# Performance work log

Hardware: AMD Instinct MI355X
Metric: run time of the kernel (lower is better)

Reference implementation:

```python
import jax, jax.numpy as jnp
import numpy as np

ATOL = 1e-06
RTOL = 1e-06

def setup_inputs() -> dict:
    key = jax.random.key(0)
    ks = jax.random.split(key, 8)
    u = lambda k, shape: jax.random.uniform(k, shape, jnp.float32, -0.05, 0.05)
    return {
        "x": jax.random.normal(ks[0], (4096, 32, 32, 3), jnp.float32),
        "W_lstm": u(ks[1], (3, 16)),      # input kernel, gates [i,f,c,o]
        "U_lstm": u(ks[2], (4, 16)),      # recurrent kernel
        "dw_kernel": u(ks[3], (27, 27, 3, 5)),  # depthwise (kh,kw,in_c,mult)
        "pw_kernel": u(ks[4], (15, 4)),   # pointwise
        "conv_bias": u(ks[5], (4,)),
        "W_td": u(ks[6], (4096, 10)),
        "W_sc": u(ks[7], (4096, 10)),
    }

def _lstm_td(x, W, U):
    # TimeDistributed LSTM: x (B,32,32,3) -> treat axis1 as TD batch, axis2 as time
    B = x.shape[0]
    seq = x.reshape(B * 32, 32, 3)          # (N, T, F)
    xs = jnp.transpose(seq, (1, 0, 2))      # (T, N, F)
    N = seq.shape[0]
    h0 = jnp.zeros((N, 4), x.dtype)
    c0 = jnp.zeros((N, 4), x.dtype)

    def step(carry, xt):
        h, c = carry
        z = xt @ W + h @ U                  # (N, 16)
        zi, zf, zc, zo = jnp.split(z, 4, axis=-1)
        i = jax.nn.elu(zi)                  # recurrent_activation='elu'
        f = jax.nn.elu(zf)
        c = f * c + i * jax.nn.softmax(zc, axis=-1)  # activation='softmax'
        o = jax.nn.elu(zo)
        h = o * jax.nn.softmax(c, axis=-1)
        return (h, c), h

    _, hs = jax.lax.scan(step, (h0, c0), xs)        # (T, N, 4)
    return jnp.transpose(hs, (1, 0, 2)).reshape(B, 32, 32, 4)

def _sep_conv(x, dw_kernel, pw_kernel, conv_bias):
    # depthwise: Keras (kh,kw,C,M) -> lax HWIO grouped (kh,kw,1,C*M), channel-major order
    dw = dw_kernel.reshape(27, 27, 1, 15)
    y = jax.lax.conv_general_dilated(
        x, dw, window_strides=(1, 1), padding='SAME',
        feature_group_count=3,
        dimension_numbers=('NHWC', 'HWIO', 'NHWC'))   # (B,32,32,15)
    y = jnp.einsum('bhwc,cf->bhwf', y, pw_kernel) + conv_bias
    return jax.nn.sigmoid(y)                          # (B,32,32,4)

def reference(x, W_lstm, U_lstm, dw_kernel, pw_kernel, conv_bias, W_td, W_sc):
    B = x.shape[0]
    td = _lstm_td(x, W_lstm, U_lstm).reshape(B, -1) @ W_td   # (B,10)
    sc = _sep_conv(x, dw_kernel, pw_kernel, conv_bias).reshape(B, -1) @ W_sc
    diff = jnp.abs(td - sc)
    tol = ATOL + RTOL * jnp.abs(sc)
    return diff <= tol
```

## Files before the change

### kernel.cpp

```cpp
#include <hip/hip_runtime.h>
#include <math.h>

#define TD_OFF 0
#define WTDR_OFF 40960
#define SC_OFF 81920
#define BG_BYTE_OFF 524288

typedef __bf16 bf16x8 __attribute__((ext_vector_type(8)));
typedef float f32x16 __attribute__((ext_vector_type(16)));

union FragU { bf16x8 v; float4 f; };

__device__ __forceinline__ f32x16 mfma16(bf16x8 a, bf16x8 b, f32x16 c) {
    return __builtin_amdgcn_mfma_f32_32x32x16_bf16(a, b, c, 0, 0, 0);
}

__device__ __forceinline__ float eluf(float v) {
    return v > 0.f ? v : __expf(v) - 1.f;
}

__global__ __launch_bounds__(256) void prep(const float* __restrict__ dw,
                                            const float* __restrict__ pw,
                                            const float* __restrict__ Wtd,
                                            float* __restrict__ Wtdr,
                                            unsigned short* __restrict__ Bg) {
    int gid = blockIdx.x * 256 + threadIdx.x;
    if (gid < 40960) {
        int k = gid & 3;
        int r = gid >> 2;
        int row = r & 31; r >>= 5;
        int j = r % 10;
        int tt = r / 10;
        Wtdr[gid] = Wtd[(size_t)(row * 128 + tt * 4 + k) * 10 + j];
        return;
    }
    int g2 = gid - 40960;
    if (g2 >= 162 * 128) return;
    int n = g2 & 127;
    int s = g2 >> 7;
    int half = s & 1;
    int cd = s >> 1;
    int c = cd / 27, d = cd % 27;
    int w = n >> 2, f = n & 3;
    unsigned short* dsth = Bg + (size_t)s * 4096 + n * 16;
    unsigned short* dstl = dsth + 2048;
#pragma unroll
    for (int k = 0; k < 16; k++) {
        int xi = half * 16 + k;
        int dx = xi - w + 13;
        float v = 0.f;
        if (dx >= 0 && dx < 27) {
#pragma unroll
            for (int m = 0; m < 5; m++)
                v = fmaf(dw[((d * 27 + dx) * 3 + c) * 5 + m],
                         pw[(c * 5 + m) * 4 + f], v);
        }
        __bf16 h = (__bf16)v;
        __bf16 l = (__bf16)(v - (float)h);
        dsth[k] = __builtin_bit_cast(unsigned short, h);
        dstl[k] = __builtin_bit_cast(unsigned short, l);
    }
}

#define A_OFF 0
#define ZOFF 49152
#define SRED_OFF 49168
#define LDS_BYTES 49488

__global__ __launch_bounds__(256, 3) void fused(const float* __restrict__ x,
                                                const float* __restrict__ W,
                                                const float* __restrict__ U,
                                                const float* __restrict__ Wtdr,
                                                const unsigned short* __restrict__ Bg,
                                                const float* __restrict__ Wsc,
                                                const float* __restrict__ bias,
                                                float* __restrict__ td_out,
                                                float* __restrict__ sc_out) {
    __shared__ char LDS[LDS_BYTES] __attribute__((aligned(16)));
    int bx = blockIdx.x;
    int rem = bx % 3;
    int q = bx / 3;
    int t = threadIdx.x;

    if (rem == 2) {
        float rW[48], rU[64];
        const float4* W4 = (const float4*)W;
        const float4* U4 = (const float4*)U;
#pragma unroll
        for (int i = 0; i < 12; i++) {
            float4 qv = W4[i];
            rW[i * 4 + 0] = qv.x; rW[i * 4 + 1] = qv.y;
            rW[i * 4 + 2] = qv.z; rW[i * 4 + 3] = qv.w;
        }
#pragma unroll
        for (int i = 0; i < 16; i++) {
            float4 qv = U4[i];
            rU[i * 4 + 0] = qv.x; rU[i * 4 + 1] = qv.y;
            rU[i * 4 + 2] = qv.z; rU[i * 4 + 3] = qv.w;
        }

        int n = q * 256 + t;
        int row = n & 31;
        const float4* xp4 = (const float4*)(x + (size_t)n * 96);

        float h0 = 0, h1 = 0, h2 = 0, h3 = 0;
        float c0 = 0, c1 = 0, c2 = 0, c3 = 0;
        float acc[10];
#pragma unroll
        for (int j = 0; j < 10; j++) acc[j] = 0.f;

        for (int g = 0; g < 8; g++) {
            float4 q0 = xp4[g * 3 + 0], q1 = xp4[g * 3 + 1], q2 = xp4[g * 3 + 2];
            float xr[12] = {q0.x, q0.y, q0.z, q0.w, q1.x, q1.y,
                            q1.z, q1.w, q2.x, q2.y, q2.z, q2.w};
#pragma unroll
            for (int st = 0; st < 4; st++) {
                int tt = g * 4 + st;
                float x0 = xr[st * 3 + 0], x1 = xr[st * 3 + 1], x2 = xr[st * 3 + 2];
                float z[16];
#pragma unroll
                for (int k = 0; k < 16; k++)
                    z[k] = x0 * rW[k] + x1 * rW[16 + k] + x2 * rW[32 + k]
                         + h0 * rU[k] + h1 * rU[16 + k] + h2 * rU[32 + k] + h3 * rU[48 + k];

                float ig0 = eluf(z[0]),  ig1 = eluf(z[1]),  ig2 = eluf(z[2]),  ig3 = eluf(z[3]);
                float fg0 = eluf(z[4]),  fg1 = eluf(z[5]),  fg2 = eluf(z[6]),  fg3 = eluf(z[7]);
                float og0 = eluf(z[12]), og1 = eluf(z[13]), og2 = eluf(z[14]), og3 = eluf(z[15]);

                float zm = fmaxf(fmaxf(z[8], z[9]), fmaxf(z[10], z[11]));
                float e0 = __expf(z[8] - zm), e1 = __expf(z[9] - zm);
                float e2 = __expf(z[10] - zm), e3 = __expf(z[11] - zm);
                float inv = 1.f / (e0 + e1 + e2 + e3);
                c0 = fg0 * c0 + ig0 * (e0 * inv);
                c1 = fg1 * c1 + ig1 * (e1 * inv);
                c2 = fg2 * c2 + ig2 * (e2 * inv);
                c3 = fg3 * c3 + ig3 * (e3 * inv);

                float cm = fmaxf(fmaxf(c0, c1), fmaxf(c2, c3));
                float p0 = __expf(c0 - cm), p1 = __expf(c1 - cm);
                float p2 = __expf(c2 - cm), p3 = __expf(c3 - cm);
                float pinv = 1.f / (p0 + p1 + p2 + p3);
                h0 = og0 * (p0 * pinv); h1 = og1 * (p1 * pinv);
                h2 = og2 * (p2 * pinv); h3 = og3 * (p3 * pinv);

                const float4* wr4 = (const float4*)(Wtdr + (size_t)tt * 1280) + row;
#pragma unroll
                for (int j = 0; j < 10; j++) {
                    float4 qv = wr4[j * 32];
                    acc[j] += h0 * qv.x + h1 * qv.y + h2 * qv.z + h3 * qv.w;
                }
            }
        }

#pragma unroll
        for (int off = 16; off >= 1; off >>= 1) {
#pragma unroll
            for (int j = 0; j < 10; j++) acc[j] += __shfl_xor(acc[j], off, 64);
        }
        int lane = t & 63;
        if (lane == 0 || lane == 32) {
            int b = n >> 5;
#pragma unroll
            for (int j = 0; j < 10; j++) td_out[b * 10 + j] = acc[j];
        }
        return;
    }

    int ci = q * 2 + rem;
    int l = t & 63;
    int wv = t >> 6;
    int m = l & 31;
    int sub = l >> 5;
    int img0 = (wv >> 1) * 2;
    int ntbase = (wv & 1) * 2;

    const char* bbase = (const char*)Bg + (size_t)ntbase * 1024 + m * 32 + sub * 16;
    FragU bufA[4], bufB[4];
#define LOADB(sv, arr) { const char* p_ = bbase + (size_t)(sv) * 8192;       \
        arr[0].f = *(const float4*)(p_);                         \
        arr[1].f = *(const float4*)(p_ + 4096);                  \
        arr[2].f = *(const float4*)(p_ + 1024);                  \
        arr[3].f = *(const float4*)(p_ + 5120); }

    LOADB(0, bufA);
    LOADB(1, bufB);

    const float4* xb4 = (const float4*)(x + (size_t)ci * 12288);
#pragma unroll
    for (int it = 0; it < 12; it++) {
        int fi = it * 256 + t;
        float4 qv = xb4[fi];
        float vals[4] = {qv.x, qv.y, qv.z, qv.w};
#pragma unroll
        for (int e = 0; e < 4; e++) {
            int pel = fi * 4 + e;
            int im = pel / 3072;
            int p = pel - im * 3072;
            int c = p % 3;
            int hw = p / 3;
            int w = hw & 31;
            int h = hw >> 5;
            int rec = A_OFF + im * 12288
                      + ((c * 8) + (w >> 4) * 2 + ((w >> 3) & 1)) * 512
                      + h * 16 + (w & 7) * 2;
            float v = vals[e];
            __bf16 hb = (__bf16)v;
            __bf16 lb = (__bf16)(v - (float)hb);
            *(__bf16*)(LDS + rec) = hb;
            *(__bf16*)(LDS + rec + 2048) = lb;
        }
    }
    if (t < 4) *(float*)(LDS + ZOFF + t * 4) = 0.f;
    __syncthreads();

    f32x16 acc00 = {0,0,0,0,0,0,0,0,0,0,0,0,0,0,0,0};
    f32x16 acc01 = acc00, acc10 = acc00, acc11 = acc00;

    int c = 0, d = 0, half = 0;

#define CHUNK(USE, SNEXT) {                                                   \
    int rowIdx = m + d - 13;                                                  \
    bool valid = (unsigned)rowIdx < 32u;                                      \
    int a0 = A_OFF + img0 * 12288 + (c * 8 + half * 2 + sub) * 512 + rowIdx * 16; \
    int ah0o = valid ? a0 : ZOFF;                                             \
    int al0o = valid ? (a0 + 2048) : ZOFF;                                    \
    int ah1o = valid ? (a0 + 12288) : ZOFF;                                   \
    int al1o = valid ? (a0 + 14336) : ZOFF;                                   \
    FragU ah0, al0, ah1, al1;                                                 \
    ah0.f = *(const float4*)(LDS + ah0o);                                     \
    al0.f = *(const float4*)(LDS + al0o);                                     \
    ah1.f = *(const float4*)(LDS + ah1o);                                     \
    al1.f = *(const float4*)(LDS + al1o);                                     \
    acc00 = mfma16(ah0.v, USE[0].v, acc00);                                   \
    acc01 = mfma16(ah0.v, USE[2].v, acc01);                                   \
    acc10 = mfma16(ah1.v, USE[0].v, acc10);                                   \
    acc11 = mfma16(ah1.v, USE[2].v, acc11);                                   \
    acc00 = mfma16(ah0.v, USE[1].v, acc00);                                   \
    acc01 = mfma16(ah0.v, USE[3].v, acc01);                                   \
    acc10 = mfma16(ah1.v, USE[1].v, acc10);                                   \
    acc11 = mfma16(ah1.v, USE[3].v, acc11);                                   \
    acc00 = mfma16(al0.v, USE[0].v, acc00);                                   \
    acc01 = mfma16(al0.v, USE[2].v, acc01);                                   \
    acc10 = mfma16(al1.v, USE[0].v, acc10);                                   \
    acc11 = mfma16(al1.v, USE[2].v, acc11);                                   \
    LOADB(SNEXT, USE);                                                        \
    half ^= 1;                                                                \
    if (!half) { d++; if (d == 27) { d = 0; c++; } }                          \
}

    for (int g = 0; g < 81; g++) {
        CHUNK(bufA, 2 * g + 2);
        CHUNK(bufB, 2 * g + 3);
    }

    float b4[4];
#pragma unroll
    for (int i = 0; i < 4; i++) b4[i] = bias[i];

    float part[2][10];
#pragma unroll
    for (int i = 0; i < 2; i++)
#pragma unroll
        for (int j = 0; j < 10; j++) part[i][j] = 0.f;

    f32x16 accs[2][2] = {{acc00, acc01}, {acc10, acc11}};
#pragma unroll
    for (int i2 = 0; i2 < 2; i2++) {
#pragma unroll
        for (int j2 = 0; j2 < 2; j2++) {
            int ncol = (ntbase + j2) * 32 + m;
            int wcol = ncol >> 2;
            int f = ncol & 3;
            f32x16 a = accs[i2][j2];
#pragma unroll
            for (int r = 0; r < 16; r++) {
                int h = (r & 3) + 8 * (r >> 2) + 4 * sub;
                float v = a[r] + b4[f];
                float sg = 1.f / (1.f + expf(-v));
                const float* wr = Wsc + (size_t)((h * 32 + wcol) * 4 + f) * 10;
#pragma unroll
                for (int j = 0; j < 10; j++) part[i2][j] = fmaf(sg, wr[j], part[i2][j]);
            }
        }
    }

#pragma unroll
    for (int off = 32; off >= 1; off >>= 1) {
#pragma unroll
        for (int i2 = 0; i2 < 2; i2++)
#pragma unroll
            for (int j = 0; j < 10; j++) part[i2][j] += __shfl_xor(part[i2][j], off, 64);
    }
    if (l == 0) {
        float* red = (float*)(LDS + SRED_OFF);
#pragma unroll
        for (int i2 = 0; i2 < 2; i2++)
#pragma unroll
            for (int j = 0; j < 10; j++) red[(wv * 2 + i2) * 10 + j] = part[i2][j];
    }
    __syncthreads();
    if (t < 40) {
        int img = t / 10, j = t % 10;
        const float* red = (const float*)(LDS + SRED_OFF);
        int pair = img >> 1, i2 = img & 1;
        float sv = red[((pair * 2) * 2 + i2) * 10 + j]
                 + red[((pair * 2 + 1) * 2 + i2) * 10 + j];
        sc_out[(ci * 4 + img) * 10 + j] = sv;
    }
}

__global__ __launch_bounds__(256) void cmp_k(const float* __restrict__ td,
                                             const float* __restrict__ sc,
                                             float* __restrict__ out) {
    int i = blockIdx.x * 256 + threadIdx.x;
    if (i < 40960) {
        float a = td[i];
        float s = sc[i];
        float tol = 1e-6f + 1e-6f * fabsf(s);
        out[i] = (fabsf(a - s) <= tol) ? 1.0f : 0.0f;
    }
}

extern "C" void kernel_launch(void* const* d_in, const int* in_sizes, int n_in,
                              void* d_out, int out_size, void* d_ws, size_t ws_size,
                              hipStream_t stream) {
    const float* x    = (const float*)d_in[0];
    const float* W    = (const float*)d_in[1];
    const float* U    = (const float*)d_in[2];
    const float* dw   = (const float*)d_in[3];
    const float* pw   = (const float*)d_in[4];
    const float* bias = (const float*)d_in[5];
    const float* Wtd  = (const float*)d_in[6];
    const float* Wsc  = (const float*)d_in[7];

    float* ws     = (float*)d_ws;
    float* td_acc = ws + TD_OFF;
    float* Wtdr   = ws + WTDR_OFF;
    float* sc_acc = ws + SC_OFF;
    unsigned short* Bg = (unsigned short*)((char*)d_ws + BG_BYTE_OFF);

    prep<<<241, 256, 0, stream>>>(dw, pw, Wtd, Wtdr, Bg);
    fused<<<1536, 256, 0, stream>>>(x, W, U, Wtdr, Bg, Wsc, bias, td_acc, sc_acc);
    cmp_k<<<160, 256, 0, stream>>>(td_acc, sc_acc, (float*)d_out);
}
```

Measured before the change: 369.3 us.

## Triple-buffer B fragments, vectorize input staging, add MFMA priority, reuse Wsc loads

New measurement: 386.0 us. +4.5%, slower.

```diff
diff --git a/kernel.cpp b/kernel.cpp
--- a/kernel.cpp
+++ b/kernel.cpp
@@ -175,7 +175,7 @@
     int ntbase = (wv & 1) * 2;
 
     const char* bbase = (const char*)Bg + (size_t)ntbase * 1024 + m * 32 + sub * 16;
-    FragU bufA[4], bufB[4];
+    FragU bufA[4], bufB[4], bufC[4];
 #define LOADB(sv, arr) { const char* p_ = bbase + (size_t)(sv) * 8192;       \
         arr[0].f = *(const float4*)(p_);                         \
         arr[1].f = *(const float4*)(p_ + 4096);                  \
@@ -184,30 +184,36 @@
 
     LOADB(0, bufA);
     LOADB(1, bufB);
-
-    const float4* xb4 = (const float4*)(x + (size_t)ci * 12288);
-#pragma unroll
-    for (int it = 0; it < 12; it++) {
-        int fi = it * 256 + t;
-        float4 qv = xb4[fi];
-        float vals[4] = {qv.x, qv.y, qv.z, qv.w};
-#pragma unroll
-        for (int e = 0; e < 4; e++) {
-            int pel = fi * 4 + e;
-            int im = pel / 3072;
-            int p = pel - im * 3072;
-            int c = p % 3;
-            int hw = p / 3;
-            int w = hw & 31;
-            int h = hw >> 5;
-            int rec = A_OFF + im * 12288
-                      + ((c * 8) + (w >> 4) * 2 + ((w >> 3) & 1)) * 512
-                      + h * 16 + (w & 7) * 2;
-            float v = vals[e];
-            __bf16 hb = (__bf16)v;
-            __bf16 lb = (__bf16)(v - (float)hb);
-            *(__bf16*)(LDS + rec) = hb;
-            *(__bf16*)(LDS + rec + 2048) = lb;
+    LOADB(2, bufC);
+
+    const float* xb = x + (size_t)ci * 12288;
+#pragma unroll
+    for (int rep = 0; rep < 2; rep++) {
+        int u = rep * 256 + t;
+        int im = u >> 7;
+        int woct = (u >> 5) & 3;
+        int h = u & 31;
+        const float4* src = (const float4*)(xb + im * 3072 + h * 96 + woct * 24);
+        float xr[24];
+#pragma unroll
+        for (int i = 0; i < 6; i++) {
+            float4 qv = src[i];
+            xr[i * 4 + 0] = qv.x; xr[i * 4 + 1] = qv.y;
+            xr[i * 4 + 2] = qv.z; xr[i * 4 + 3] = qv.w;
+        }
+#pragma unroll
+        for (int c = 0; c < 3; c++) {
+            FragU hiF, loF;
+#pragma unroll
+            for (int k = 0; k < 8; k++) {
+                float v = xr[k * 3 + c];
+                __bf16 hb = (__bf16)v;
+                hiF.v[k] = hb;
+                loF.v[k] = (__bf16)(v - (float)hb);
+            }
+            int rec = A_OFF + im * 12288 + (c * 8 + woct) * 512 + h * 16;
+            *(float4*)(LDS + rec) = hiF.f;
+            *(float4*)(LDS + rec + 2048) = loF.f;
         }
     }
     if (t < 4) *(float*)(LDS + ZOFF + t * 4) = 0.f;
@@ -222,15 +228,12 @@
     int rowIdx = m + d - 13;                                                  \
     bool valid = (unsigned)rowIdx < 32u;                                      \
     int a0 = A_OFF + img0 * 12288 + (c * 8 + half * 2 + sub) * 512 + rowIdx * 16; \
-    int ah0o = valid ? a0 : ZOFF;                                             \
-    int al0o = valid ? (a0 + 2048) : ZOFF;                                    \
-    int ah1o = valid ? (a0 + 12288) : ZOFF;                                   \
-    int al1o = valid ? (a0 + 14336) : ZOFF;                                   \
     FragU ah0, al0, ah1, al1;                                                 \
-    ah0.f = *(const float4*)(LDS + ah0o);                                     \
-    al0.f = *(const float4*)(LDS + al0o);                                     \
-    ah1.f = *(const float4*)(LDS + ah1o);                                     \
-    al1.f = *(const float4*)(LDS + al1o);                                     \
+    ah0.f = *(const float4*)(LDS + (valid ? a0           : ZOFF));            \
+    al0.f = *(const float4*)(LDS + (valid ? a0 + 2048    : ZOFF));            \
+    ah1.f = *(const float4*)(LDS + (valid ? a0 + 12288   : ZOFF));            \
+    al1.f = *(const float4*)(LDS + (valid ? a0 + 14336   : ZOFF));            \
+    __builtin_amdgcn_s_setprio(1);                                            \
     acc00 = mfma16(ah0.v, USE[0].v, acc00);                                   \
     acc01 = mfma16(ah0.v, USE[2].v, acc01);                                   \
     acc10 = mfma16(ah1.v, USE[0].v, acc10);                                   \
@@ -243,14 +246,16 @@
     acc01 = mfma16(al0.v, USE[2].v, acc01);                                   \
     acc10 = mfma16(al1.v, USE[0].v, acc10);                                   \
     acc11 = mfma16(al1.v, USE[2].v, acc11);                                   \
+    __builtin_amdgcn_s_setprio(0);                                            \
     LOADB(SNEXT, USE);                                                        \
     half ^= 1;                                                                \
     if (!half) { d++; if (d == 27) { d = 0; c++; } }                          \
 }
 
-    for (int g = 0; g < 81; g++) {
-        CHUNK(bufA, 2 * g + 2);
-        CHUNK(bufB, 2 * g + 3);
+    for (int g = 0; g < 54; g++) {
+        CHUNK(bufA, 3 * g + 3);
+        CHUNK(bufB, 3 * g + 4);
+        CHUNK(bufC, 3 * g + 5);
     }
 
     float b4[4];
@@ -265,21 +270,23 @@
 
     f32x16 accs[2][2] = {{acc00, acc01}, {acc10, acc11}};
 #pragma unroll
-    for (int i2 = 0; i2 < 2; i2++) {
-#pragma unroll
-        for (int j2 = 0; j2 < 2; j2++) {
-            int ncol = (ntbase + j2) * 32 + m;
-            int wcol = ncol >> 2;
-            int f = ncol & 3;
-            f32x16 a = accs[i2][j2];
-#pragma unroll
-            for (int r = 0; r < 16; r++) {
-                int h = (r & 3) + 8 * (r >> 2) + 4 * sub;
-                float v = a[r] + b4[f];
+    for (int j2 = 0; j2 < 2; j2++) {
+        int ncol = (ntbase + j2) * 32 + m;
+        int wcol = ncol >> 2;
+        int f = ncol & 3;
+#pragma unroll
+        for (int r = 0; r < 16; r++) {
+            int h = (r & 3) + 8 * (r >> 2) + 4 * sub;
+            const float* wr = Wsc + (size_t)((h * 32 + wcol) * 4 + f) * 10;
+            float wreg[10];
+#pragma unroll
+            for (int j = 0; j < 10; j++) wreg[j] = wr[j];
+#pragma unroll
+            for (int i2 = 0; i2 < 2; i2++) {
+                float v = accs[i2][j2][r] + b4[f];
                 float sg = 1.f / (1.f + expf(-v));
-                const float* wr = Wsc + (size_t)((h * 32 + wcol) * 4 + f) * 10;
-#pragma unroll
-                for (int j = 0; j < 10; j++) part[i2][j] = fmaf(sg, wr[j], part[i2][j]);
+#pragma unroll
+                for (int j = 0; j < 10; j++) part[i2][j] = fmaf(sg, wreg[j], part[i2][j]);
             }
         }
     }
```
